# Kernel tuning notes

Measured on AMD Instinct MI355X. Metric: run time of the kernel, lower is better.

The kernel has to match this reference:

```python
import jax, jax.numpy as jnp
import numpy as np

NUM_EMBEDDINGS = 1024
EMBEDDING_DIM = 512
B, H, W = 32, 32, 32


def setup_inputs() -> dict:
    key = jax.random.key(0)
    k1, k2 = jax.random.split(key)
    z = jax.random.normal(k1, (B, EMBEDDING_DIM, H, W), dtype=jnp.float32)
    embedding = jax.random.normal(k2, (NUM_EMBEDDINGS, EMBEDDING_DIM), dtype=jnp.float32)
    return {"z": z, "embedding": embedding}


def reference(z, embedding):
    # z: [B, C, H, W] -> [B, H, W, C] -> [N, C]
    zp = jnp.transpose(z, (0, 2, 3, 1))
    b, h, w, d = zp.shape
    z_flat = zp.reshape(-1, d)
    # squared L2 distances: ||z||^2 - 2 z e^T + ||e||^2  -> [N, K]
    distances = (
        jnp.sum(z_flat ** 2, axis=1, keepdims=True)
        - 2.0 * (z_flat @ embedding.T)
        + jnp.sum(embedding ** 2, axis=1)
    )
    indices = jnp.argmin(distances, axis=1)  # [N]
    # one-hot @ embedding == direct gather
    quantized = embedding[indices]  # [N, d]
    quantized = quantized.reshape(b, h, w, d).transpose(0, 3, 1, 2)  # [B, C, H, W]
    return quantized, 0.0, indices.reshape(b, -1)
```

## Files before the change

kernel.cpp:

```cpp
#include <hip/hip_runtime.h>
#include <cfloat>

typedef _Float16 half8 __attribute__((ext_vector_type(8)));
typedef float    f32x4 __attribute__((ext_vector_type(4)));
typedef unsigned int  uint;
typedef unsigned short ushort;

constexpr int DIM  = 512;
constexpr int NEMB = 1024;
constexpr int HW   = 1024;
constexpr int NROW = 32 * HW;

constexpr long long QCOUNT = (long long)32 * 512 * 32 * 32;
constexpr long long SOFF   = QCOUNT;
constexpr long long IOFF   = SOFF + 1;

constexpr size_t WS_ZT    = 0;
constexpr size_t WS_ET    = 33554432;
constexpr size_t WS_ENORM = 34603008;
constexpr size_t WS_CNT   = 34607104;
constexpr size_t WS_LIST  = 34607360;
constexpr size_t WS_CANDB = WS_LIST + (size_t)NROW * 4;
constexpr size_t WS_CANDI = WS_CANDB + (size_t)2 * NROW * 8;
constexpr size_t WS_NEED  = WS_CANDI + (size_t)2 * NROW * 4;

constexpr float DELTA = 0.25f;

__device__ __forceinline__ void gld16(const void* g, void* l) {
    __builtin_amdgcn_global_load_lds(
        (const __attribute__((address_space(1))) void*)g,
        (__attribute__((address_space(3))) void*)l, 16, 0, 0);
}
union PKH8 { half8 v; _Float16 h[8]; };

__device__ __forceinline__ int swz8(int r, int g) {
    return g ^ (r & 7);
}

__global__ __launch_bounds__(256) void eprep(const float* __restrict__ e,
                                             char* __restrict__ et,
                                             float* __restrict__ enorm,
                                             int* __restrict__ cnt) {
    if (blockIdx.x == 0 && threadIdx.x == 0) *cnt = 0;
    int gid = blockIdx.x * 256 + threadIdx.x;
    int ke  = gid >> 6;
    int kbg = gid & 63;
    const float* src = e + (size_t)ke * DIM + kbg * 8;
    PKH8 h;
    float s = 0.f;
    #pragma unroll
    for (int j = 0; j < 8; ++j) {
        float v = src[j];
        h.h[j] = (_Float16)v;
        s += v * v;
    }
    int nc = ke >> 7, r = ke & 127, kc64 = kbg >> 3, g = kbg & 7;
    size_t byte = ((size_t)(nc * 8 + kc64)) * 16384 + (size_t)r * 128
                + ((size_t)swz8(r, g) << 4);
    *reinterpret_cast<half8*>(et + byte) = h.v;
    #pragma unroll
    for (int off = 32; off > 0; off >>= 1) s += __shfl_down(s, off, 64);
    if (kbg == 0) enorm[ke] = s;
}

__global__ __launch_bounds__(256) void zprep(const float* __restrict__ z,
                                             char* __restrict__ zt) {
    __shared__ float ls[64][129];
    const int bx  = blockIdx.x;
    const int mb  = bx >> 3, kcc = bx & 7;
    const int b   = mb >> 3;
    const int hw0 = (mb & 7) * 128;
    const int t = threadIdx.x;
    for (int i = t; i < 64 * 128; i += 256) {
        int c = i >> 7, hw = i & 127;
        ls[c][hw] = z[((size_t)(b * DIM + kcc * 64 + c)) * HW + hw0 + hw];
    }
    __syncthreads();
    for (int j = t; j < 1024; j += 256) {
        int r = j >> 3, g = j & 7;
        PKH8 h;
        #pragma unroll
        for (int jj = 0; jj < 8; ++jj) h.h[jj] = (_Float16)ls[g * 8 + jj][r];
        size_t byte = ((size_t)(mb * 8 + kcc)) * 16384 + (size_t)r * 128
                    + ((size_t)swz8(r, g) << 4);
        *reinterpret_cast<half8*>(zt + byte) = h.v;
    }
}

#define VQ_STAGE(SS, BUF)                                                      \
  {                                                                            \
    const int kc_ = (SS) & 7;                                                  \
    const size_t tB_ = ((size_t)((half4 + ((SS) >> 3)) * 8 + kc_)) * 16384;    \
    char* dst_ = smem + (BUF) * 32768;                                         \
    gld16(zt + zbase + (size_t)kc_ * 16384 + toff,        dst_ + toff);        \
    gld16(zt + zbase + (size_t)kc_ * 16384 + 8192 + toff, dst_ + 8192 + toff); \
    gld16(et + tB_ + toff,        dst_ + 16384 + toff);                        \
    gld16(et + tB_ + 8192 + toff, dst_ + 24576 + toff);                        \
  }

#define VQ_STEP(S, VMLIT, BUF)                                                 \
  {                                                                            \
    asm volatile("s_waitcnt vmcnt(" VMLIT ")" ::: "memory");                   \
    __builtin_amdgcn_s_barrier();                                              \
    const char* buf_ = smem + (BUF) * 32768;                                   \
    half8 a00 = *reinterpret_cast<const half8*>(buf_ + aoff0);                 \
    half8 a01 = *reinterpret_cast<const half8*>(buf_ + aoff1);                 \
    half8 a10 = *reinterpret_cast<const half8*>(buf_ + (aoff0 ^ 64));          \
    half8 a11 = *reinterpret_cast<const half8*>(buf_ + (aoff1 ^ 64));          \
    half8 b00 = *reinterpret_cast<const half8*>(buf_ + 16384 + boff0);         \
    half8 b01 = *reinterpret_cast<const half8*>(buf_ + 16384 + boff1);         \
    half8 b02 = *reinterpret_cast<const half8*>(buf_ + 16384 + boff2);         \
    half8 b03 = *reinterpret_cast<const half8*>(buf_ + 16384 + boff3);         \
    half8 b10 = *reinterpret_cast<const half8*>(buf_ + 16384 + (boff0 ^ 64));  \
    half8 b11 = *reinterpret_cast<const half8*>(buf_ + 16384 + (boff1 ^ 64));  \
    half8 b12 = *reinterpret_cast<const half8*>(buf_ + 16384 + (boff2 ^ 64));  \
    half8 b13 = *reinterpret_cast<const half8*>(buf_ + 16384 + (boff3 ^ 64));  \
    asm volatile("s_waitcnt lgkmcnt(0)" ::: "memory");                         \
    __builtin_amdgcn_sched_barrier(0);                                         \
    __builtin_amdgcn_s_barrier();                                              \
    if ((S) + 2 < 32) VQ_STAGE((S) + 2, BUF);                                  \
    acc[0][0] = __builtin_amdgcn_mfma_f32_16x16x32_f16(a00, b00, acc[0][0], 0, 0, 0); \
    acc[0][1] = __builtin_amdgcn_mfma_f32_16x16x32_f16(a00, b01, acc[0][1], 0, 0, 0); \
    acc[0][2] = __builtin_amdgcn_mfma_f32_16x16x32_f16(a00, b02, acc[0][2], 0, 0, 0); \
    acc[0][3] = __builtin_amdgcn_mfma_f32_16x16x32_f16(a00, b03, acc[0][3], 0, 0, 0); \
    acc[1][0] = __builtin_amdgcn_mfma_f32_16x16x32_f16(a01, b00, acc[1][0], 0, 0, 0); \
    acc[1][1] = __builtin_amdgcn_mfma_f32_16x16x32_f16(a01, b01, acc[1][1], 0, 0, 0); \
    acc[1][2] = __builtin_amdgcn_mfma_f32_16x16x32_f16(a01, b02, acc[1][2], 0, 0, 0); \
    acc[1][3] = __builtin_amdgcn_mfma_f32_16x16x32_f16(a01, b03, acc[1][3], 0, 0, 0); \
    acc[0][0] = __builtin_amdgcn_mfma_f32_16x16x32_f16(a10, b10, acc[0][0], 0, 0, 0); \
    acc[0][1] = __builtin_amdgcn_mfma_f32_16x16x32_f16(a10, b11, acc[0][1], 0, 0, 0); \
    acc[0][2] = __builtin_amdgcn_mfma_f32_16x16x32_f16(a10, b12, acc[0][2], 0, 0, 0); \
    acc[0][3] = __builtin_amdgcn_mfma_f32_16x16x32_f16(a10, b13, acc[0][3], 0, 0, 0); \
    acc[1][0] = __builtin_amdgcn_mfma_f32_16x16x32_f16(a11, b10, acc[1][0], 0, 0, 0); \
    acc[1][1] = __builtin_amdgcn_mfma_f32_16x16x32_f16(a11, b11, acc[1][1], 0, 0, 0); \
    acc[1][2] = __builtin_amdgcn_mfma_f32_16x16x32_f16(a11, b12, acc[1][2], 0, 0, 0); \
    acc[1][3] = __builtin_amdgcn_mfma_f32_16x16x32_f16(a11, b13, acc[1][3], 0, 0, 0); \
    if (((S) & 7) == 7) {                                                      \
      const int ncl_ = ((S) >> 3) * 128;                                       \
      _Pragma("unroll")                                                        \
      for (int n = 0; n < 4; ++n) {                                            \
        const int lcol = ncl_ + wc * 64 + n * 16 + lr;                         \
        const float en = enorm_l[lcol];                                        \
        const int col = half * 512 + lcol;                                     \
        _Pragma("unroll")                                                      \
        for (int m = 0; m < 2; ++m) {                                          \
          _Pragma("unroll")                                                    \
          for (int q = 0; q < 4; ++q) {                                        \
            float dv = en - 2.0f * acc[m][n][q];                               \
            int sl = m * 4 + q;                                                \
            if (dv < b1v[sl]) { b2v[sl] = b1v[sl]; b1v[sl] = dv; i1v[sl] = col; } \
            else if (dv < b2v[sl]) b2v[sl] = dv;                               \
          }                                                                    \
        }                                                                      \
      }                                                                        \
      _Pragma("unroll")                                                        \
      for (int m = 0; m < 2; ++m)                                              \
        _Pragma("unroll")                                                      \
        for (int n = 0; n < 4; ++n) acc[m][n] = (f32x4)(0.f);                  \
    }                                                                          \
  }

__global__ __launch_bounds__(512, 4) void vq_mfma(const char* __restrict__ zt,
                                                  const char* __restrict__ et,
                                                  const float* __restrict__ enorm,
                                                  float2* __restrict__ cand_b,
                                                  int* __restrict__ cand_i) {
    __shared__ __align__(16) char smem[65536];
    __shared__ float enorm_l[512];

    const int t = threadIdx.x;
    const int w = t >> 6, l = t & 63;
    const int lr = l & 15, hg = l >> 4;
    const int wr = w >> 1;
    const int wc = w & 1;
    const int bid = blockIdx.x;
    const int mb = bid >> 1;
    const int half = bid & 1;
    const int half4 = half * 4;
    const int n0 = mb * 128;

    const int swz = swz8(lr, hg) << 4;
    const int aoff0 = (wr * 32 + lr) * 128 + swz;
    const int aoff1 = (wr * 32 + 16 + lr) * 128 + swz;
    const int boff0 = (wc * 64 + lr) * 128 + swz;
    const int boff1 = (wc * 64 + 16 + lr) * 128 + swz;
    const int boff2 = (wc * 64 + 32 + lr) * 128 + swz;
    const int boff3 = (wc * 64 + 48 + lr) * 128 + swz;

    enorm_l[t] = enorm[half * 512 + t];
    __syncthreads();

    float b1v[8], b2v[8]; int i1v[8];
    #pragma unroll
    for (int s = 0; s < 8; ++s) { b1v[s] = FLT_MAX; b2v[s] = FLT_MAX; i1v[s] = 0; }

    const size_t zbase = (size_t)mb * 8 * 16384;
    const int toff = t * 16;

    f32x4 acc[2][4];
    #pragma unroll
    for (int m = 0; m < 2; ++m)
        #pragma unroll
        for (int n = 0; n < 4; ++n) acc[m][n] = (f32x4)(0.f);

    VQ_STAGE(0, 0);
    VQ_STAGE(1, 1);

    for (int sp = 0; sp < 30; sp += 2) {
        VQ_STEP(sp + 0, "4", 0);
        VQ_STEP(sp + 1, "4", 1);
    }
    VQ_STEP(30, "4", 0);
    VQ_STEP(31, "0", 1);

    #pragma unroll
    for (int s = 0; s < 8; ++s) {
        #pragma unroll
        for (int off = 1; off <= 8; off <<= 1) {
            float ob1 = __shfl_xor(b1v[s], off, 64);
            int   oi1 = __shfl_xor(i1v[s], off, 64);
            float ob2 = __shfl_xor(b2v[s], off, 64);
            if (ob1 < b1v[s] || (ob1 == b1v[s] && oi1 < i1v[s])) {
                b2v[s] = fminf(b1v[s], ob2);
                b1v[s] = ob1; i1v[s] = oi1;
            } else {
                b2v[s] = fminf(b2v[s], ob1);
            }
        }
    }
    __syncthreads();
    float* red_b1 = reinterpret_cast<float*>(smem);
    float* red_b2 = reinterpret_cast<float*>(smem + 1024);
    int*   red_i1 = reinterpret_cast<int*>  (smem + 2048);
    if (lr == 0) {
        #pragma unroll
        for (int s = 0; s < 8; ++s) {
            int row = wr * 32 + (s >> 2) * 16 + hg * 4 + (s & 3);
            red_b1[row * 2 + wc] = b1v[s];
            red_b2[row * 2 + wc] = b2v[s];
            red_i1[row * 2 + wc] = i1v[s];
        }
    }
    __syncthreads();
    if (t < 128) {
        float a1 = red_b1[t * 2], a2 = red_b2[t * 2]; int ai = red_i1[t * 2];
        float c1 = red_b1[t * 2 + 1], c2 = red_b2[t * 2 + 1]; int ci = red_i1[t * 2 + 1];
        float B1, B2; int I1;
        if (c1 < a1 || (c1 == a1 && ci < ai)) { B1 = c1; I1 = ci; B2 = fminf(a1, c2); }
        else                                   { B1 = a1; I1 = ai; B2 = fminf(a2, c1); }
        cand_b[(size_t)half * NROW + n0 + t] = make_float2(B1, B2);
        cand_i[(size_t)half * NROW + n0 + t] = I1;
    }
}

__global__ __launch_bounds__(256) void combine(const float2* __restrict__ cand_b,
                                               const int* __restrict__ cand_i,
                                               const float* __restrict__ e,
                                               float* __restrict__ out,
                                               int* __restrict__ cnt,
                                               int* __restrict__ list) {
    __shared__ int idx_f[64];
    const int t = threadIdx.x;
    const int n0 = blockIdx.x * 64;
    if (t < 64) {
        const int row = n0 + t;
        float2 a = cand_b[row];
        float2 c = cand_b[NROW + row];
        int ai = cand_i[row];
        int ci = cand_i[NROW + row];
        float B1, B2; int I1;
        if (c.x < a.x) { B1 = c.x; I1 = ci; B2 = fminf(a.x, c.y); }
        else           { B1 = a.x; I1 = ai; B2 = fminf(a.y, c.x); }
        idx_f[t] = I1;
        out[IOFF + row] = (float)I1;
        if (B2 - B1 < DELTA) {
            int pos = atomicAdd(cnt, 1);
            list[pos] = row;
        }
    }
    if (blockIdx.x == 0 && t == 0) out[SOFF] = 0.0f;
    __syncthreads();

    const int b   = n0 >> 10;
    const int hw0 = n0 & (HW - 1);
    const int row4 = (t & 15) * 4;
    const int i0 = idx_f[row4 + 0];
    const int i1 = idx_f[row4 + 1];
    const int i2 = idx_f[row4 + 2];
    const int i3 = idx_f[row4 + 3];
    #pragma unroll 4
    for (int p = 0; p < 32; ++p) {
        int c = (t >> 4) + (p << 4);
        float4 v;
        v.x = e[(size_t)i0 * DIM + c];
        v.y = e[(size_t)i1 * DIM + c];
        v.z = e[(size_t)i2 * DIM + c];
        v.w = e[(size_t)i3 * DIM + c];
        *reinterpret_cast<float4*>(&out[((size_t)(b * DIM + c)) * HW + hw0 + row4]) = v;
    }
}

__global__ __launch_bounds__(256) void recheck(const float* __restrict__ z,
                                               const float* __restrict__ e,
                                               const float* __restrict__ enorm,
                                               const int* __restrict__ cnt,
                                               const int* __restrict__ list,
                                               float* __restrict__ out) {
    __shared__ float zrow[4][512];
    __shared__ float rb[256];
    __shared__ int   ri[256];
    __shared__ int   fidx[4];
    const int t = threadIdx.x;
    const int count = *cnt;
    const int ngrp = (count + 3) >> 2;
    for (int g = blockIdx.x; g < ngrp; g += gridDim.x) {
        const int base = g * 4;
        const int nr = min(4, count - base);
        __syncthreads();
        for (int r = 0; r < nr; ++r) {
            const int row = list[base + r];
            const int b = row >> 10, hw = row & (HW - 1);
            zrow[r][t]       = z[((size_t)(b * DIM + t))       * HW + hw];
            zrow[r][t + 256] = z[((size_t)(b * DIM + t + 256)) * HW + hw];
        }
        __syncthreads();
        float best[4]; int bi[4];
        #pragma unroll
        for (int r = 0; r < 4; ++r) { best[r] = FLT_MAX; bi[r] = 0; }
        #pragma unroll
        for (int p = 0; p < 4; ++p) {
            const int ke = t + p * 256;
            const float4* ep = reinterpret_cast<const float4*>(e + (size_t)ke * DIM);
            float d0 = 0.f, d1 = 0.f, d2 = 0.f, d3 = 0.f;
            const float4* z0 = reinterpret_cast<const float4*>(zrow[0]);
            const float4* z1 = reinterpret_cast<const float4*>(zrow[1]);
            const float4* z2 = reinterpret_cast<const float4*>(zrow[2]);
            const float4* z3 = reinterpret_cast<const float4*>(zrow[3]);
            for (int c = 0; c < 128; ++c) {
                float4 ev = ep[c];
                float4 a0 = z0[c], a1 = z1[c], a2 = z2[c], a3 = z3[c];
                d0 += ev.x*a0.x + ev.y*a0.y + ev.z*a0.z + ev.w*a0.w;
                d1 += ev.x*a1.x + ev.y*a1.y + ev.z*a1.z + ev.w*a1.w;
                d2 += ev.x*a2.x + ev.y*a2.y + ev.z*a2.z + ev.w*a2.w;
                d3 += ev.x*a3.x + ev.y*a3.y + ev.z*a3.z + ev.w*a3.w;
            }
            const float en = enorm[ke];
            float dd[4] = { en - 2.f*d0, en - 2.f*d1, en - 2.f*d2, en - 2.f*d3 };
            #pragma unroll
            for (int r = 0; r < 4; ++r)
                if (dd[r] < best[r]) { best[r] = dd[r]; bi[r] = ke; }
        }
        for (int r = 0; r < nr; ++r) {
            rb[t] = best[r]; ri[t] = bi[r];
            __syncthreads();
            #pragma unroll
            for (int s = 128; s > 0; s >>= 1) {
                if (t < s) {
                    float ov = rb[t + s]; int oi = ri[t + s];
                    if (ov < rb[t] || (ov == rb[t] && oi < ri[t])) {
                        rb[t] = ov; ri[t] = oi;
                    }
                }
                __syncthreads();
            }
            if (t == 0) {
                fidx[r] = ri[0];
                out[IOFF + list[base + r]] = (float)ri[0];
            }
            __syncthreads();
        }
        for (int r = 0; r < nr; ++r) {
            const int row = list[base + r];
            const int b = row >> 10, hw = row & (HW - 1);
            const int fbi = fidx[r];
            out[((size_t)(b * DIM + t))       * HW + hw] = e[(size_t)fbi * DIM + t];
            out[((size_t)(b * DIM + t + 256)) * HW + hw] = e[(size_t)fbi * DIM + t + 256];
        }
    }
}

constexpr int TM = 64;
constexpr int TN = 256;
constexpr int KC = 32;
constexpr int ZST = 68;
constexpr int EST = 260;

union F4 { float4 v; float f[4]; };

__global__ __launch_bounds__(256) void enorm_kernel(const float* __restrict__ e,
                                                    float* __restrict__ enorm) {
    int gid  = blockIdx.x * 256 + threadIdx.x;
    int wave = gid >> 6;
    int lane = gid & 63;
    if (wave >= NEMB) return;
    const float* row = e + (size_t)wave * DIM;
    float4 a = *reinterpret_cast<const float4*>(row + lane * 8);
    float4 b = *reinterpret_cast<const float4*>(row + lane * 8 + 4);
    float s = a.x*a.x + a.y*a.y + a.z*a.z + a.w*a.w
            + b.x*b.x + b.y*b.y + b.z*b.z + b.w*b.w;
    #pragma unroll
    for (int off = 32; off > 0; off >>= 1) s += __shfl_down(s, off, 64);
    if (lane == 0) enorm[wave] = s;
}

__global__ __launch_bounds__(256) void vq_main_kernel(const float* __restrict__ z,
                                                      const float* __restrict__ e,
                                                      const float* __restrict__ enorm,
                                                      float* __restrict__ out) {
    __shared__ float zs[KC][ZST];
    __shared__ float es[KC][EST];
    __shared__ float enorm_l[NEMB];
    __shared__ int   idx_f[TM];

    const int t   = threadIdx.x;
    const int n0  = blockIdx.x * TM;
    const int b   = n0 >> 10;
    const int hw0 = n0 & (HW - 1);
    const float* zb = z + ((size_t)b * DIM) * HW + hw0;

    #pragma unroll
    for (int i = 0; i < 4; ++i) enorm_l[t + i * 256] = enorm[t + i * 256];

    const int rg = t >> 5;
    const int cg = t & 31;

    float best[8];
    int   bidx[8];
    #pragma unroll
    for (int i = 0; i < 8; ++i) { best[i] = FLT_MAX; bidx[i] = 0; }

    const int z_r4 = (t & 15) * 4;
    const int z_c  = t >> 4;
    const int e_ke = t >> 3;
    const int e_c4 = t & 7;

    for (int nc = 0; nc < NEMB / TN; ++nc) {
        const int k0 = nc * TN;
        float acc[8][8];
        #pragma unroll
        for (int mi = 0; mi < 8; ++mi)
            #pragma unroll
            for (int nj = 0; nj < 8; ++nj) acc[mi][nj] = 0.f;

        for (int kc = 0; kc < DIM / KC; ++kc) {
            const int c0 = kc * KC;
            __syncthreads();
            #pragma unroll
            for (int p = 0; p < 2; ++p) {
                int c = z_c + p * 16;
                float4 v = *reinterpret_cast<const float4*>(zb + (size_t)(c0 + c) * HW + z_r4);
                *reinterpret_cast<float4*>(&zs[c][z_r4]) = v;
            }
            #pragma unroll
            for (int p = 0; p < 8; ++p) {
                int ke = e_ke + p * 32;
                float4 v = *reinterpret_cast<const float4*>(e + (size_t)(k0 + ke) * DIM + c0 + e_c4 * 4);
                es[e_c4 * 4 + 0][ke] = v.x;
                es[e_c4 * 4 + 1][ke] = v.y;
                es[e_c4 * 4 + 2][ke] = v.z;
                es[e_c4 * 4 + 3][ke] = v.w;
            }
            __syncthreads();
            #pragma unroll
            for (int kk = 0; kk < KC; ++kk) {
                F4 zf0, zf1, ef0, ef1;
                zf0.v = *reinterpret_cast<const float4*>(&zs[kk][rg * 8]);
                zf1.v = *reinterpret_cast<const float4*>(&zs[kk][rg * 8 + 4]);
                ef0.v = *reinterpret_cast<const float4*>(&es[kk][cg * 4]);
                ef1.v = *reinterpret_cast<const float4*>(&es[kk][128 + cg * 4]);
                #pragma unroll
                for (int mi = 0; mi < 4; ++mi) {
                    #pragma unroll
                    for (int nj = 0; nj < 4; ++nj) {
                        acc[mi][nj]         += zf0.f[mi] * ef0.f[nj];
                        acc[mi][nj + 4]     += zf0.f[mi] * ef1.f[nj];
                        acc[mi + 4][nj]     += zf1.f[mi] * ef0.f[nj];
                        acc[mi + 4][nj + 4] += zf1.f[mi] * ef1.f[nj];
                    }
                }
            }
        }
        #pragma unroll
        for (int mi = 0; mi < 8; ++mi) {
            #pragma unroll
            for (int nj = 0; nj < 8; ++nj) {
                int col = k0 + (nj < 4 ? cg * 4 + nj : 128 + cg * 4 + (nj - 4));
                float dv = enorm_l[col] - 2.0f * acc[mi][nj];
                if (dv < best[mi]) { best[mi] = dv; bidx[mi] = col; }
            }
        }
    }

    __syncthreads();
    float* best_l = reinterpret_cast<float*>(es);
    int*   idx_l  = reinterpret_cast<int*>(reinterpret_cast<char*>(es) + (size_t)TM * 33 * 4);
    #pragma unroll
    for (int mi = 0; mi < 8; ++mi) {
        int row = rg * 8 + mi;
        best_l[row * 33 + cg] = best[mi];
        idx_l[row * 33 + cg]  = bidx[mi];
    }
    __syncthreads();
    if (t < TM) {
        float bv = best_l[t * 33];
        int   bi = idx_l[t * 33];
        #pragma unroll
        for (int c = 1; c < 32; ++c) {
            float v  = best_l[t * 33 + c];
            int   ix = idx_l[t * 33 + c];
            if (v < bv || (v == bv && ix < bi)) { bv = v; bi = ix; }
        }
        idx_f[t] = bi;
        out[IOFF + n0 + t] = (float)bi;
    }
    if (blockIdx.x == 0 && t == 0) out[SOFF] = 0.0f;
    __syncthreads();

    const int row4 = (t & 15) * 4;
    const int i0 = idx_f[row4 + 0];
    const int i1 = idx_f[row4 + 1];
    const int i2 = idx_f[row4 + 2];
    const int i3 = idx_f[row4 + 3];
    #pragma unroll 4
    for (int p = 0; p < 32; ++p) {
        int c = (t >> 4) + (p << 4);
        float4 v;
        v.x = e[(size_t)i0 * DIM + c];
        v.y = e[(size_t)i1 * DIM + c];
        v.z = e[(size_t)i2 * DIM + c];
        v.w = e[(size_t)i3 * DIM + c];
        *reinterpret_cast<float4*>(&out[((size_t)(b * DIM + c)) * HW + hw0 + row4]) = v;
    }
}

extern "C" void kernel_launch(void* const* d_in, const int* in_sizes, int n_in,
                              void* d_out, int out_size, void* d_ws, size_t ws_size,
                              hipStream_t stream) {
    const float* z = (const float*)d_in[0];
    const float* e = (const float*)d_in[1];
    float* out = (float*)d_out;
    char*  ws  = (char*)d_ws;

    if (ws_size >= WS_NEED) {
        char*   zt     = ws + WS_ZT;
        char*   et     = ws + WS_ET;
        float*  enorm  = (float*)(ws + WS_ENORM);
        int*    cnt    = (int*)(ws + WS_CNT);
        int*    list   = (int*)(ws + WS_LIST);
        float2* cand_b = (float2*)(ws + WS_CANDB);
        int*    cand_i = (int*)(ws + WS_CANDI);

        hipLaunchKernelGGL(eprep,   dim3(256),            dim3(256), 0, stream, e, et, enorm, cnt);
        hipLaunchKernelGGL(zprep,   dim3(2048),           dim3(256), 0, stream, z, zt);
        hipLaunchKernelGGL(vq_mfma, dim3(NROW / 128 * 2), dim3(512), 0, stream,
                           zt, et, enorm, cand_b, cand_i);
        hipLaunchKernelGGL(combine, dim3(NROW / 64),      dim3(256), 0, stream,
                           cand_b, cand_i, e, out, cnt, list);
        hipLaunchKernelGGL(recheck, dim3(1024),           dim3(256), 0, stream,
                           z, e, enorm, cnt, list, out);
    } else {
        float* enorm = (float*)ws;
        hipLaunchKernelGGL(enorm_kernel,   dim3(NEMB / 4), dim3(256), 0, stream, e, enorm);
        hipLaunchKernelGGL(vq_main_kernel, dim3(NROW / TM), dim3(256), 0, stream,
                           z, e, enorm, out);
    }
}
```

Baseline: 218.3 us.

## Fuse combine into VQ GEMM with full-codebook blocks and resident Z tile

The VQ MFMA kernel now handles all 1024 codebook entries per 128-row block instead of splitting them across two blocks. This removes the candidate buffers and the separate combine kernel, so the argmin, flag list and gather/transpose output are done in the same kernel. The whole 128x512 fp16 Z tile is loaded into 128KB of LDS once and only the codebook tiles are double-buffered. The -0.5*||e||^2 term is folded into the accumulator initialisation to save the per-chunk epilogue arithmetic. In exchange the grid drops to 256 blocks of 512 threads with 160KB LDS each, which lowers occupancy and leaves much less parallelism on the GPU.

```diff
diff --git a/kernel.cpp b/kernel.cpp
--- a/kernel.cpp
+++ b/kernel.cpp
@@ -20,9 +20,7 @@
 constexpr size_t WS_ENORM = 34603008;
 constexpr size_t WS_CNT   = 34607104;
 constexpr size_t WS_LIST  = 34607360;
-constexpr size_t WS_CANDB = WS_LIST + (size_t)NROW * 4;
-constexpr size_t WS_CANDI = WS_CANDB + (size_t)2 * NROW * 8;
-constexpr size_t WS_NEED  = WS_CANDI + (size_t)2 * NROW * 4;
+constexpr size_t WS_NEED  = WS_LIST + (size_t)NROW * 4;
 
 constexpr float DELTA = 0.25f;
 
@@ -87,38 +85,36 @@
     }
 }
 
-#define VQ_STAGE(SS, BUF)                                                      \
+#define VQ_STAGE_B(T_)                                                         \
   {                                                                            \
-    const int kc_ = (SS) & 7;                                                  \
-    const size_t tB_ = ((size_t)((half4 + ((SS) >> 3)) * 8 + kc_)) * 16384;    \
-    char* dst_ = smem + (BUF) * 32768;                                         \
-    gld16(zt + zbase + (size_t)kc_ * 16384 + toff,        dst_ + toff);        \
-    gld16(zt + zbase + (size_t)kc_ * 16384 + 8192 + toff, dst_ + 8192 + toff); \
-    gld16(et + tB_ + toff,        dst_ + 16384 + toff);                        \
-    gld16(et + tB_ + 8192 + toff, dst_ + 24576 + toff);                        \
+    gld16(et + (size_t)(T_) * 16384 + toff,                                    \
+          smem + 131072 + ((T_) & 1) * 16384 + toff);                          \
+    gld16(et + (size_t)(T_) * 16384 + 8192 + toff,                             \
+          smem + 131072 + ((T_) & 1) * 16384 + 8192 + toff);                   \
   }
 
-#define VQ_STEP(S, VMLIT, BUF)                                                 \
+#define VQ_STEP(NC, KC, VMLIT)                                                 \
   {                                                                            \
     asm volatile("s_waitcnt vmcnt(" VMLIT ")" ::: "memory");                   \
     __builtin_amdgcn_s_barrier();                                              \
-    const char* buf_ = smem + (BUF) * 32768;                                   \
-    half8 a00 = *reinterpret_cast<const half8*>(buf_ + aoff0);                 \
-    half8 a01 = *reinterpret_cast<const half8*>(buf_ + aoff1);                 \
-    half8 a10 = *reinterpret_cast<const half8*>(buf_ + (aoff0 ^ 64));          \
-    half8 a11 = *reinterpret_cast<const half8*>(buf_ + (aoff1 ^ 64));          \
-    half8 b00 = *reinterpret_cast<const half8*>(buf_ + 16384 + boff0);         \
-    half8 b01 = *reinterpret_cast<const half8*>(buf_ + 16384 + boff1);         \
-    half8 b02 = *reinterpret_cast<const half8*>(buf_ + 16384 + boff2);         \
-    half8 b03 = *reinterpret_cast<const half8*>(buf_ + 16384 + boff3);         \
-    half8 b10 = *reinterpret_cast<const half8*>(buf_ + 16384 + (boff0 ^ 64));  \
-    half8 b11 = *reinterpret_cast<const half8*>(buf_ + 16384 + (boff1 ^ 64));  \
-    half8 b12 = *reinterpret_cast<const half8*>(buf_ + 16384 + (boff2 ^ 64));  \
-    half8 b13 = *reinterpret_cast<const half8*>(buf_ + 16384 + (boff3 ^ 64));  \
+    const char* abuf_ = smem + (KC) * 16384;                                   \
+    const char* bbuf_ = smem + 131072 + (((NC) * 8 + (KC)) & 1) * 16384;       \
+    half8 a00 = *reinterpret_cast<const half8*>(abuf_ + aoff0);                \
+    half8 a01 = *reinterpret_cast<const half8*>(abuf_ + aoff1);                \
+    half8 a10 = *reinterpret_cast<const half8*>(abuf_ + (aoff0 ^ 64));         \
+    half8 a11 = *reinterpret_cast<const half8*>(abuf_ + (aoff1 ^ 64));         \
+    half8 b00 = *reinterpret_cast<const half8*>(bbuf_ + boff0);                \
+    half8 b01 = *reinterpret_cast<const half8*>(bbuf_ + boff1);                \
+    half8 b02 = *reinterpret_cast<const half8*>(bbuf_ + boff2);                \
+    half8 b03 = *reinterpret_cast<const half8*>(bbuf_ + boff3);                \
+    half8 b10 = *reinterpret_cast<const half8*>(bbuf_ + (boff0 ^ 64));         \
+    half8 b11 = *reinterpret_cast<const half8*>(bbuf_ + (boff1 ^ 64));         \
+    half8 b12 = *reinterpret_cast<const half8*>(bbuf_ + (boff2 ^ 64));         \
+    half8 b13 = *reinterpret_cast<const half8*>(bbuf_ + (boff3 ^ 64));         \
     asm volatile("s_waitcnt lgkmcnt(0)" ::: "memory");                         \
     __builtin_amdgcn_sched_barrier(0);                                         \
     __builtin_amdgcn_s_barrier();                                              \
-    if ((S) + 2 < 32) VQ_STAGE((S) + 2, BUF);                                  \
+    if ((NC) * 8 + (KC) + 2 < 64) VQ_STAGE_B((NC) * 8 + (KC) + 2);             \
     acc[0][0] = __builtin_amdgcn_mfma_f32_16x16x32_f16(a00, b00, acc[0][0], 0, 0, 0); \
     acc[0][1] = __builtin_amdgcn_mfma_f32_16x16x32_f16(a00, b01, acc[0][1], 0, 0, 0); \
     acc[0][2] = __builtin_amdgcn_mfma_f32_16x16x32_f16(a00, b02, acc[0][2], 0, 0, 0); \
@@ -135,48 +131,51 @@
     acc[1][1] = __builtin_amdgcn_mfma_f32_16x16x32_f16(a11, b11, acc[1][1], 0, 0, 0); \
     acc[1][2] = __builtin_amdgcn_mfma_f32_16x16x32_f16(a11, b12, acc[1][2], 0, 0, 0); \
     acc[1][3] = __builtin_amdgcn_mfma_f32_16x16x32_f16(a11, b13, acc[1][3], 0, 0, 0); \
-    if (((S) & 7) == 7) {                                                      \
-      const int ncl_ = ((S) >> 3) * 128;                                       \
+  }
+
+#define VQ_CHUNK(NC, L6, L7)                                                   \
+  {                                                                            \
+    _Pragma("unroll")                                                          \
+    for (int n = 0; n < 4; ++n) {                                              \
+      f32x4 iv = (f32x4)(env[(NC) * 4 + n]);                                   \
+      acc[0][n] = iv; acc[1][n] = iv;                                          \
+    }                                                                          \
+  }                                                                            \
+  VQ_STEP(NC, 0, "2") VQ_STEP(NC, 1, "2") VQ_STEP(NC, 2, "2")                  \
+  VQ_STEP(NC, 3, "2") VQ_STEP(NC, 4, "2") VQ_STEP(NC, 5, "2")                  \
+  VQ_STEP(NC, 6, L6)  VQ_STEP(NC, 7, L7)                                       \
+  {                                                                            \
+    _Pragma("unroll")                                                          \
+    for (int n = 0; n < 4; ++n) {                                              \
+      const int col = (NC) * 128 + wc * 64 + n * 16 + lr;                      \
       _Pragma("unroll")                                                        \
-      for (int n = 0; n < 4; ++n) {                                            \
-        const int lcol = ncl_ + wc * 64 + n * 16 + lr;                         \
-        const float en = enorm_l[lcol];                                        \
-        const int col = half * 512 + lcol;                                     \
+      for (int m = 0; m < 2; ++m) {                                            \
         _Pragma("unroll")                                                      \
-        for (int m = 0; m < 2; ++m) {                                          \
-          _Pragma("unroll")                                                    \
-          for (int q = 0; q < 4; ++q) {                                        \
-            float dv = en - 2.0f * acc[m][n][q];                               \
-            int sl = m * 4 + q;                                                \
-            if (dv < b1v[sl]) { b2v[sl] = b1v[sl]; b1v[sl] = dv; i1v[sl] = col; } \
-            else if (dv < b2v[sl]) b2v[sl] = dv;                               \
-          }                                                                    \
+        for (int q = 0; q < 4; ++q) {                                          \
+          float dv = -2.0f * acc[m][n][q];                                     \
+          int sl = m * 4 + q;                                                  \
+          if (dv < b1v[sl]) { b2v[sl] = b1v[sl]; b1v[sl] = dv; i1v[sl] = col; }\
+          else if (dv < b2v[sl]) b2v[sl] = dv;                                 \
         }                                                                      \
       }                                                                        \
-      _Pragma("unroll")                                                        \
-      for (int m = 0; m < 2; ++m)                                              \
-        _Pragma("unroll")                                                      \
-        for (int n = 0; n < 4; ++n) acc[m][n] = (f32x4)(0.f);                  \
     }                                                                          \
   }
 
-__global__ __launch_bounds__(512, 4) void vq_mfma(const char* __restrict__ zt,
+__global__ __launch_bounds__(512, 2) void vq_mfma(const char* __restrict__ zt,
                                                   const char* __restrict__ et,
                                                   const float* __restrict__ enorm,
-                                                  float2* __restrict__ cand_b,
-                                                  int* __restrict__ cand_i) {
-    __shared__ __align__(16) char smem[65536];
-    __shared__ float enorm_l[512];
+                                                  const float* __restrict__ e,
+                                                  float* __restrict__ out,
+                                                  int* __restrict__ cnt,
+                                                  int* __restrict__ list) {
+    __shared__ __align__(16) char smem[163840];
 
     const int t = threadIdx.x;
     const int w = t >> 6, l = t & 63;
     const int lr = l & 15, hg = l >> 4;
     const int wr = w >> 1;
     const int wc = w & 1;
-    const int bid = blockIdx.x;
-    const int mb = bid >> 1;
-    const int half = bid & 1;
-    const int half4 = half * 4;
+    const int mb = blockIdx.x;
     const int n0 = mb * 128;
 
     const int swz = swz8(lr, hg) << 4;
@@ -187,31 +186,38 @@
     const int boff2 = (wc * 64 + 32 + lr) * 128 + swz;
     const int boff3 = (wc * 64 + 48 + lr) * 128 + swz;
 
-    enorm_l[t] = enorm[half * 512 + t];
-    __syncthreads();
+    float env[32];
+    #pragma unroll
+    for (int nc = 0; nc < 8; ++nc)
+        #pragma unroll
+        for (int n = 0; n < 4; ++n)
+            env[nc * 4 + n] = -0.5f * enorm[nc * 128 + wc * 64 + n * 16 + lr];
 
     float b1v[8], b2v[8]; int i1v[8];
     #pragma unroll
     for (int s = 0; s < 8; ++s) { b1v[s] = FLT_MAX; b2v[s] = FLT_MAX; i1v[s] = 0; }
 
-    const size_t zbase = (size_t)mb * 8 * 16384;
+    __syncthreads();
+
+    const size_t zbase = (size_t)mb * 131072;
     const int toff = t * 16;
 
     f32x4 acc[2][4];
-    #pragma unroll
-    for (int m = 0; m < 2; ++m)
-        #pragma unroll
-        for (int n = 0; n < 4; ++n) acc[m][n] = (f32x4)(0.f);
-
-    VQ_STAGE(0, 0);
-    VQ_STAGE(1, 1);
-
-    for (int sp = 0; sp < 30; sp += 2) {
-        VQ_STEP(sp + 0, "4", 0);
-        VQ_STEP(sp + 1, "4", 1);
-    }
-    VQ_STEP(30, "4", 0);
-    VQ_STEP(31, "0", 1);
+
+    #pragma unroll
+    for (int i = 0; i < 16; ++i)
+        gld16(zt + zbase + (size_t)i * 8192 + toff, smem + i * 8192 + toff);
+    VQ_STAGE_B(0);
+    VQ_STAGE_B(1);
+
+    VQ_CHUNK(0, "2", "2")
+    VQ_CHUNK(1, "2", "2")
+    VQ_CHUNK(2, "2", "2")
+    VQ_CHUNK(3, "2", "2")
+    VQ_CHUNK(4, "2", "2")
+    VQ_CHUNK(5, "2", "2")
+    VQ_CHUNK(6, "2", "2")
+    VQ_CHUNK(7, "2", "0")
 
     #pragma unroll
     for (int s = 0; s < 8; ++s) {
@@ -232,6 +238,7 @@
     float* red_b1 = reinterpret_cast<float*>(smem);
     float* red_b2 = reinterpret_cast<float*>(smem + 1024);
     int*   red_i1 = reinterpret_cast<int*>  (smem + 2048);
+    int*   idx_f  = reinterpret_cast<int*>  (smem + 3072);
     if (lr == 0) {
         #pragma unroll
         for (int s = 0; s < 8; ++s) {
@@ -248,54 +255,32 @@
         float B1, B2; int I1;
         if (c1 < a1 || (c1 == a1 && ci < ai)) { B1 = c1; I1 = ci; B2 = fminf(a1, c2); }
         else                                   { B1 = a1; I1 = ai; B2 = fminf(a2, c1); }
-        cand_b[(size_t)half * NROW + n0 + t] = make_float2(B1, B2);
-        cand_i[(size_t)half * NROW + n0 + t] = I1;
-    }
-}
-
-__global__ __launch_bounds__(256) void combine(const float2* __restrict__ cand_b,
-                                               const int* __restrict__ cand_i,
-                                               const float* __restrict__ e,
-                                               float* __restrict__ out,
-                                               int* __restrict__ cnt,
-                                               int* __restrict__ list) {
-    __shared__ int idx_f[64];
-    const int t = threadIdx.x;
-    const int n0 = blockIdx.x * 64;
-    if (t < 64) {
-        const int row = n0 + t;
-        float2 a = cand_b[row];
-        float2 c = cand_b[NROW + row];
-        int ai = cand_i[row];
-        int ci = cand_i[NROW + row];
-        float B1, B2; int I1;
-        if (c.x < a.x) { B1 = c.x; I1 = ci; B2 = fminf(a.x, c.y); }
-        else           { B1 = a.x; I1 = ai; B2 = fminf(a.y, c.x); }
         idx_f[t] = I1;
-        out[IOFF + row] = (float)I1;
+        out[IOFF + n0 + t] = (float)I1;
         if (B2 - B1 < DELTA) {
             int pos = atomicAdd(cnt, 1);
-            list[pos] = row;
-        }
-    }
-    if (blockIdx.x == 0 && t == 0) out[SOFF] = 0.0f;
-    __syncthreads();
-
-    const int b   = n0 >> 10;
-    const int hw0 = n0 & (HW - 1);
-    const int row4 = (t & 15) * 4;
+            list[pos] = n0 + t;
+        }
+    }
+    if (mb == 0 && t == 0) out[SOFF] = 0.0f;
+    __syncthreads();
+
+    const int b   = mb >> 3;
+    const int hw0 = (mb & 7) * 128;
+    const int row4 = (t & 31) * 4;
     const int i0 = idx_f[row4 + 0];
-    const int i1 = idx_f[row4 + 1];
+    const int i1g = idx_f[row4 + 1];
     const int i2 = idx_f[row4 + 2];
     const int i3 = idx_f[row4 + 3];
+    const int cbase = t >> 5;
     #pragma unroll 4
     for (int p = 0; p < 32; ++p) {
-        int c = (t >> 4) + (p << 4);
+        int c = cbase + (p << 4);
         float4 v;
-        v.x = e[(size_t)i0 * DIM + c];
-        v.y = e[(size_t)i1 * DIM + c];
-        v.z = e[(size_t)i2 * DIM + c];
-        v.w = e[(size_t)i3 * DIM + c];
+        v.x = e[(size_t)i0  * DIM + c];
+        v.y = e[(size_t)i1g * DIM + c];
+        v.z = e[(size_t)i2  * DIM + c];
+        v.w = e[(size_t)i3  * DIM + c];
         *reinterpret_cast<float4*>(&out[((size_t)(b * DIM + c)) * HW + hw0 + row4]) = v;
     }
 }
@@ -547,16 +532,12 @@
         float*  enorm  = (float*)(ws + WS_ENORM);
         int*    cnt    = (int*)(ws + WS_CNT);
         int*    list   = (int*)(ws + WS_LIST);
-        float2* cand_b = (float2*)(ws + WS_CANDB);
-        int*    cand_i = (int*)(ws + WS_CANDI);
-
-        hipLaunchKernelGGL(eprep,   dim3(256),            dim3(256), 0, stream, e, et, enorm, cnt);
-        hipLaunchKernelGGL(zprep,   dim3(2048),           dim3(256), 0, stream, z, zt);
-        hipLaunchKernelGGL(vq_mfma, dim3(NROW / 128 * 2), dim3(512), 0, stream,
-                           zt, et, enorm, cand_b, cand_i);
-        hipLaunchKernelGGL(combine, dim3(NROW / 64),      dim3(256), 0, stream,
-                           cand_b, cand_i, e, out, cnt, list);
-        hipLaunchKernelGGL(recheck, dim3(1024),           dim3(256), 0, stream,
+
+        hipLaunchKernelGGL(eprep,   dim3(256),  dim3(256), 0, stream, e, et, enorm, cnt);
+        hipLaunchKernelGGL(zprep,   dim3(2048), dim3(256), 0, stream, z, zt);
+        hipLaunchKernelGGL(vq_mfma, dim3(256),  dim3(512), 0, stream,
+                           zt, et, enorm, e, out, cnt, list);
+        hipLaunchKernelGGL(recheck, dim3(1024), dim3(256), 0, stream,
                            z, e, enorm, cnt, list, out);
     } else {
         float* enorm = (float*)ws;
```

Result: slower. 264.2 us (+21.0%).
